# Performance work log

Measured on AMD Instinct MI355X. Metric: run time of the kernel, lower is better.

Reference implementation:

```python
import jax, jax.numpy as jnp
import numpy as np

B, C, E, H = 4, 2048, 1024, 16
D = E // H
EPS = 1e-5

def _layernorm(x, g, b):
    mu = jnp.mean(x, axis=-1, keepdims=True)
    var = jnp.mean(jnp.square(x - mu), axis=-1, keepdims=True)
    return (x - mu) * jax.lax.rsqrt(var + EPS) * g + b

def setup_inputs() -> dict:
    key = jax.random.key(0)
    ks = jax.random.split(key, 12)
    s = 1.0 / np.sqrt(E)
    return {
        "inputs": jax.random.normal(ks[0], (B, C, E), dtype=jnp.float32),
        "Wq": jax.random.normal(ks[1], (E, E), dtype=jnp.float32) * s,
        "bq": jnp.zeros((E,), dtype=jnp.float32),
        "Wk": jax.random.normal(ks[2], (E, E), dtype=jnp.float32) * s,
        "bk": jnp.zeros((E,), dtype=jnp.float32),
        "Wv": jax.random.normal(ks[3], (E, E), dtype=jnp.float32) * s,
        "bv": jnp.zeros((E,), dtype=jnp.float32),
        "g1": jnp.ones((E,), dtype=jnp.float32),
        "beta1": jnp.zeros((E,), dtype=jnp.float32),
        "g2": jnp.ones((E,), dtype=jnp.float32),
        "beta2": jnp.zeros((E,), dtype=jnp.float32),
        "W1": jax.random.normal(ks[4], (E, 4 * E), dtype=jnp.float32) * s,
        "bm1": jnp.zeros((4 * E,), dtype=jnp.float32),
        "W2": jax.random.normal(ks[5], (4 * E, E), dtype=jnp.float32) * (1.0 / np.sqrt(4 * E)),
        "bm2": jnp.zeros((E,), dtype=jnp.float32),
    }

def reference(inputs, Wq, bq, Wk, bk, Wv, bv, g1, beta1, g2, beta2, W1, bm1, W2, bm2):
    b, c, e = inputs.shape
    normed = _layernorm(inputs, g1, beta1)
    q = (normed @ Wq + bq).reshape(b, c, H, D).transpose(0, 2, 1, 3)  # [B,H,C,D]
    k = (normed @ Wk + bk).reshape(b, c, H, D).transpose(0, 2, 1, 3)
    v = (normed @ Wv + bv).reshape(b, c, H, D).transpose(0, 2, 1, 3)
    scores = jnp.einsum('bhqd,bhkd->bhqk', q, k) / np.sqrt(D).astype(np.float32)
    causal = jnp.triu(jnp.ones((c, c), dtype=bool), k=1)  # True above diagonal
    scores = jnp.where(causal, -jnp.inf, scores)
    probs = jax.nn.softmax(scores, axis=-1)
    attn = jnp.einsum('bhqk,bhkd->bhqd', probs, v)
    attn = attn.transpose(0, 2, 1, 3).reshape(b, c, e)
    out = inputs + attn
    h = _layernorm(out, g2, beta2)
    mlp = jax.nn.relu(h @ W1 + bm1) @ W2 + bm2
    return out + mlp
```

## Files before the change

kernel.cpp:

```cpp
#include <hip/hip_runtime.h>
#include <math.h>

#define B_ 4
#define C_ 2048
#define E_ 1024
#define H_ 16
#define D_ 64
#define ROWS_ (B_*C_)

typedef __bf16 bf16x8 __attribute__((ext_vector_type(8)));
typedef float f32x4 __attribute__((ext_vector_type(4)));

__device__ __forceinline__ float b2f(unsigned short u) {
  unsigned int x = ((unsigned int)u) << 16;
  return __builtin_bit_cast(float, x);
}
__device__ __forceinline__ unsigned short f2b(float f) {
  unsigned int x = __builtin_bit_cast(unsigned int, f);
  unsigned int r = (x + 0x7FFFu + ((x >> 16) & 1u)) >> 16;
  return (unsigned short)r;
}
__device__ __forceinline__ unsigned short tob(float f) { return f2b(f); }
__device__ __forceinline__ unsigned short tob(unsigned short u) { return u; }
__device__ __forceinline__ void store_out(float* p, float v) { *p = v; }
__device__ __forceinline__ void store_out(unsigned short* p, float v) { *p = f2b(v); }

__device__ __forceinline__ void async16(const void* g, void* l) {
  __builtin_amdgcn_global_load_lds(
      (__attribute__((address_space(1))) unsigned int*)g,
      (__attribute__((address_space(3))) unsigned int*)l, 16, 0, 0);
}

template <typename InT>
__global__ __launch_bounds__(256) void transpose64(
    const InT* __restrict__ in, unsigned short* __restrict__ out,
    int s_in, int s_out, int Hz, long zs_b, long zs_h, long zs_out)
{
  __shared__ unsigned short t[64][65];
  int z = blockIdx.z;
  long ib = (long)(z / Hz) * zs_b + (long)(z % Hz) * zs_h;
  long ob = (long)z * zs_out;
  int r0 = blockIdx.y * 64, c0 = blockIdx.x * 64;
  int lane = threadIdx.x & 63, grp = threadIdx.x >> 6;
  for (int i = grp; i < 64; i += 4)
    t[i][lane] = tob(in[ib + (long)(r0 + i) * s_in + c0 + lane]);
  __syncthreads();
  for (int i = grp; i < 64; i += 4)
    out[ob + (long)(c0 + i) * s_out + r0 + lane] = t[lane][i];
}

__global__ void concat_bias(const float* __restrict__ q,
                            const float* __restrict__ k,
                            const float* __restrict__ v,
                            float* __restrict__ o)
{
  int i = blockIdx.x * 256 + threadIdx.x;
  o[i] = (i < 1024) ? q[i] : (i < 2048) ? k[i - 1024] : v[i - 2048];
}

__global__ __launch_bounds__(256) void ln_kernel(
    const float* __restrict__ xin, const unsigned short* __restrict__ addend,
    const float* __restrict__ g, const float* __restrict__ beta,
    unsigned short* __restrict__ yout, float* __restrict__ out1)
{
  int row = blockIdx.x, tid = threadIdx.x;
  size_t base = (size_t)row * E_ + tid * 4;
  float4 xa = *(const float4*)(xin + base);
  float v0 = xa.x, v1 = xa.y, v2 = xa.z, v3 = xa.w;
  if (addend) {
    ushort4 aa = *(const ushort4*)(addend + base);
    v0 += b2f(aa.x); v1 += b2f(aa.y); v2 += b2f(aa.z); v3 += b2f(aa.w);
  }
  if (out1) {
    *(float4*)(out1 + base) = make_float4(v0, v1, v2, v3);
  }
  float s = v0 + v1 + v2 + v3;
  float sq = v0*v0 + v1*v1 + v2*v2 + v3*v3;
  #pragma unroll
  for (int off = 32; off >= 1; off >>= 1) {
    s  += __shfl_xor(s, off);
    sq += __shfl_xor(sq, off);
  }
  __shared__ float red[8];
  int wid = tid >> 6;
  if ((tid & 63) == 0) { red[wid] = s; red[4 + wid] = sq; }
  __syncthreads();
  s  = red[0] + red[1] + red[2] + red[3];
  sq = red[4] + red[5] + red[6] + red[7];
  float mu = s * (1.0f / E_);
  float var = sq * (1.0f / E_) - mu * mu;
  float rs = rsqrtf(var + 1e-5f);
  float4 ga = *(const float4*)(g + tid * 4);
  float4 ba = *(const float4*)(beta + tid * 4);
  ushort4 o;
  o.x = f2b((v0 - mu) * rs * ga.x + ba.x);
  o.y = f2b((v1 - mu) * rs * ga.y + ba.y);
  o.z = f2b((v2 - mu) * rs * ga.z + ba.z);
  o.w = f2b((v3 - mu) * rs * ga.w + ba.w);
  *(ushort4*)(yout + base) = o;
}

template <typename OutT>
__global__ __launch_bounds__(256) void gemm_bt(
    const unsigned short* __restrict__ A, const unsigned short* __restrict__ Bt,
    const float* __restrict__ bias, const float* __restrict__ resid,
    OutT* __restrict__ Co, int M, int N, int K, int relu)
{
  __shared__ __align__(16) unsigned short As[128 * 32];
  __shared__ __align__(16) unsigned short Bs[128 * 32];
  int tid = threadIdx.x, lane = tid & 63, wid = tid >> 6;
  int lane15 = lane & 15, quad = lane >> 4;
  int bn = blockIdx.x, bm = blockIdx.y;
  int m_lo = (wid & 1) * 64, n_lo = (wid >> 1) * 64;

  f32x4 acc[4][4];
  #pragma unroll
  for (int i = 0; i < 4; ++i)
    #pragma unroll
    for (int j = 0; j < 4; ++j) acc[i][j] = 0.0f;

  int c0 = wid * 64 + lane;
  int kc8 = (c0 & 3) * 8;
  const unsigned short* Ag0 = A  + (size_t)(bm * 128 + (c0 >> 2)) * K + kc8;
  const unsigned short* Ag1 = A  + (size_t)(bm * 128 + (c0 >> 2) + 64) * K + kc8;
  const unsigned short* Bg0 = Bt + (size_t)(bn * 128 + (c0 >> 2)) * K + kc8;
  const unsigned short* Bg1 = Bt + (size_t)(bn * 128 + (c0 >> 2) + 64) * K + kc8;
  unsigned short* As0 = &As[(wid * 64) * 8];
  unsigned short* As1 = &As[(256 + wid * 64) * 8];
  unsigned short* Bs0 = &Bs[(wid * 64) * 8];
  unsigned short* Bs1 = &Bs[(256 + wid * 64) * 8];

  for (int k0 = 0; k0 < K; k0 += 32) {
    async16(Ag0 + k0, As0);
    async16(Ag1 + k0, As1);
    async16(Bg0 + k0, Bs0);
    async16(Bg1 + k0, Bs1);
    __syncthreads();
    bf16x8 af[4], bfr[4];
    #pragma unroll
    for (int t = 0; t < 4; ++t)
      af[t] = *(const bf16x8*)&As[(m_lo + t * 16 + lane15) * 32 + quad * 8];
    #pragma unroll
    for (int t = 0; t < 4; ++t)
      bfr[t] = *(const bf16x8*)&Bs[(n_lo + t * 16 + lane15) * 32 + quad * 8];
    #pragma unroll
    for (int mt = 0; mt < 4; ++mt)
      #pragma unroll
      for (int nt = 0; nt < 4; ++nt)
        acc[mt][nt] = __builtin_amdgcn_mfma_f32_16x16x32_bf16(af[mt], bfr[nt], acc[mt][nt], 0, 0, 0);
    __syncthreads();
  }

  #pragma unroll
  for (int nt = 0; nt < 4; ++nt) {
    int col = bn * 128 + n_lo + nt * 16 + lane15;
    float bv = bias[col];
    #pragma unroll
    for (int mt = 0; mt < 4; ++mt) {
      int row0 = bm * 128 + m_lo + mt * 16 + quad * 4;
      #pragma unroll
      for (int r = 0; r < 4; ++r) {
        float val = acc[mt][nt][r] + bv;
        if (relu) val = fmaxf(val, 0.0f);
        if (resid) val += resid[(size_t)(row0 + r) * N + col];
        store_out(&Co[(size_t)(row0 + r) * N + col], val);
      }
    }
  }
}

__global__ __launch_bounds__(512) void attn_kernel(
    const unsigned short* __restrict__ qkv, const unsigned short* __restrict__ vt,
    unsigned short* __restrict__ attnb)
{
  __shared__ __align__(16) unsigned short Klds[64 * 64];
  __shared__ __align__(16) unsigned short Vlds[64 * 64];
  __shared__ __align__(16) unsigned short Plds[8][16 * 72];
  int tid = threadIdx.x, lane = tid & 63, widx = tid >> 6;
  int lane15 = lane & 15, quad = lane >> 4;
  int qblk = 15 - blockIdx.x;
  int bh = blockIdx.y;
  int b = bh >> 4, h = bh & 15;
  int q0w = qblk * 128 + widx * 16;

  const float QSCALE = 0.18033688011112042f;
  const unsigned short* qb = qkv + (size_t)(b * C_ + q0w + lane15) * 3072 + h * 64;
  bf16x8 qa0 = *(const bf16x8*)(qb + quad * 8);
  bf16x8 qa1 = *(const bf16x8*)(qb + 32 + quad * 8);
  #pragma unroll
  for (int j = 0; j < 8; ++j) {
    qa0[j] = (__bf16)((float)qa0[j] * QSCALE);
    qa1[j] = (__bf16)((float)qa1[j] * QSCALE);
  }

  float lsum[4];
  f32x4 o[4];
  #pragma unroll
  for (int r = 0; r < 4; ++r) lsum[r] = 0.0f;
  #pragma unroll
  for (int nt = 0; nt < 4; ++nt) o[nt] = 0.0f;

  int sr = tid >> 3, sc = tid & 7, sw = sr & 7;
  const unsigned short* kg = qkv + (size_t)(b * C_ + sr) * 3072 + 1024 + h * 64 + (sc ^ sw) * 8;
  const unsigned short* vg = vt + (size_t)bh * 64 * 2048 + (size_t)sr * 2048 + (sc ^ sw) * 8;
  unsigned short* kl = &Klds[sr * 64 + sc * 8];
  unsigned short* vl = &Vlds[sr * 64 + sc * 8];
  int swr = lane15 & 7;

  int ntiles = 2 * qblk + 2;
  for (int kt = 0; kt < ntiles; ++kt) {
    int k0 = kt * 64;
    async16(kg, kl);
    async16(vg, vl);
    kg += (size_t)64 * 3072;
    vg += 64;
    __syncthreads();

    if (k0 <= q0w + 15) {
      f32x4 s[4];
      #pragma unroll
      for (int g = 0; g < 4; ++g) s[g] = 0.0f;
      #pragma unroll
      for (int g = 0; g < 4; ++g) {
        int row = g * 16 + lane15;
        bf16x8 kf0 = *(const bf16x8*)&Klds[row * 64 + ((quad ^ swr) * 8)];
        bf16x8 kf1 = *(const bf16x8*)&Klds[row * 64 + (((4 + quad) ^ swr) * 8)];
        s[g] = __builtin_amdgcn_mfma_f32_16x16x32_bf16(qa0, kf0, s[g], 0, 0, 0);
        s[g] = __builtin_amdgcn_mfma_f32_16x16x32_bf16(qa1, kf1, s[g], 0, 0, 0);
      }

      if (k0 + 63 > q0w) {
        #pragma unroll
        for (int g = 0; g < 4; ++g)
          #pragma unroll
          for (int r = 0; r < 4; ++r)
            if (k0 + g * 16 + lane15 > q0w + quad * 4 + r) s[g][r] = -3.0e38f;
      }

      float p[4][4];
      #pragma unroll
      for (int g = 0; g < 4; ++g)
        #pragma unroll
        for (int r = 0; r < 4; ++r) p[g][r] = exp2f(s[g][r]);
      #pragma unroll
      for (int r = 0; r < 4; ++r)
        lsum[r] += (p[0][r] + p[1][r]) + (p[2][r] + p[3][r]);

      __bf16* prow = (__bf16*)&Plds[widx][0];
      #pragma unroll
      for (int g = 0; g < 4; ++g)
        #pragma unroll
        for (int r = 0; r < 4; ++r)
          prow[(quad * 4 + r) * 72 + g * 16 + lane15] = (__bf16)p[g][r];
      asm volatile("s_waitcnt lgkmcnt(0)" ::: "memory");
      bf16x8 pa0 = *(const bf16x8*)&Plds[widx][lane15 * 72 + quad * 8];
      bf16x8 pa1 = *(const bf16x8*)&Plds[widx][lane15 * 72 + 32 + quad * 8];

      #pragma unroll
      for (int nt = 0; nt < 4; ++nt) {
        int d = nt * 16 + lane15;
        bf16x8 vf0 = *(const bf16x8*)&Vlds[d * 64 + ((quad ^ swr) * 8)];
        bf16x8 vf1 = *(const bf16x8*)&Vlds[d * 64 + (((4 + quad) ^ swr) * 8)];
        o[nt] = __builtin_amdgcn_mfma_f32_16x16x32_bf16(pa0, vf0, o[nt], 0, 0, 0);
        o[nt] = __builtin_amdgcn_mfma_f32_16x16x32_bf16(pa1, vf1, o[nt], 0, 0, 0);
      }
    }
    __syncthreads();
  }

  #pragma unroll
  for (int off = 1; off <= 8; off <<= 1)
    #pragma unroll
    for (int r = 0; r < 4; ++r)
      lsum[r] += __shfl_xor(lsum[r], off);
  float rl[4];
  #pragma unroll
  for (int r = 0; r < 4; ++r) rl[r] = 1.0f / lsum[r];

  #pragma unroll
  for (int nt = 0; nt < 4; ++nt) {
    #pragma unroll
    for (int r = 0; r < 4; ++r) {
      float val = o[nt][r] * rl[r];
      attnb[(size_t)(b * C_ + q0w + quad * 4 + r) * E_ + h * 64 + nt * 16 + lane15] = f2b(val);
    }
  }
}

extern "C" void kernel_launch(void* const* d_in, const int* in_sizes, int n_in,
                              void* d_out, int out_size, void* d_ws, size_t ws_size,
                              hipStream_t stream)
{
  const float* x   = (const float*)d_in[0];
  const float* Wq  = (const float*)d_in[1];
  const float* bq  = (const float*)d_in[2];
  const float* Wk  = (const float*)d_in[3];
  const float* bk  = (const float*)d_in[4];
  const float* Wv  = (const float*)d_in[5];
  const float* bv  = (const float*)d_in[6];
  const float* g1  = (const float*)d_in[7];
  const float* be1 = (const float*)d_in[8];
  const float* g2  = (const float*)d_in[9];
  const float* be2 = (const float*)d_in[10];
  const float* W1  = (const float*)d_in[11];
  const float* bm1 = (const float*)d_in[12];
  const float* W2  = (const float*)d_in[13];
  const float* bm2 = (const float*)d_in[14];

  char* ws = (char*)d_ws;
  unsigned short* norm1 = (unsigned short*)(ws + 0);
  unsigned short* wT    = (unsigned short*)(ws + 16777216);
  unsigned short* w1T   = (unsigned short*)(ws + 23068672);
  unsigned short* w2T   = (unsigned short*)(ws + 31457280);
  float*          biasq = (float*)(ws + 39845888);
  unsigned short* qkv   = (unsigned short*)(ws + 39858176);
  unsigned short* vtb   = (unsigned short*)(ws + 90189824);
  unsigned short* mid   = (unsigned short*)(ws + 39858176);
  unsigned short* attnb = (unsigned short*)(ws + 106967040);
  float*          out1  = (float*)(ws + 123744256);

  transpose64<float><<<dim3(16, 16, 1), 256, 0, stream>>>(Wq, wT,               1024, 1024, 1, 0, 0, 0);
  transpose64<float><<<dim3(16, 16, 1), 256, 0, stream>>>(Wk, wT + 1024 * 1024, 1024, 1024, 1, 0, 0, 0);
  transpose64<float><<<dim3(16, 16, 1), 256, 0, stream>>>(Wv, wT + 2048 * 1024, 1024, 1024, 1, 0, 0, 0);
  transpose64<float><<<dim3(64, 16, 1), 256, 0, stream>>>(W1, w1T, 4096, 1024, 1, 0, 0, 0);
  transpose64<float><<<dim3(16, 64, 1), 256, 0, stream>>>(W2, w2T, 1024, 4096, 1, 0, 0, 0);
  concat_bias<<<12, 256, 0, stream>>>(bq, bk, bv, biasq);

  ln_kernel<<<ROWS_, 256, 0, stream>>>(x, nullptr, g1, be1, norm1, nullptr);

  gemm_bt<unsigned short><<<dim3(24, 64), 256, 0, stream>>>(
      norm1, wT, biasq, nullptr, qkv, 8192, 3072, 1024, 0);

  transpose64<unsigned short><<<dim3(1, 32, 64), 256, 0, stream>>>(
      qkv + 2048, vtb, 3072, 2048, 16, (long)C_ * 3072, 64, (long)64 * 2048);

  attn_kernel<<<dim3(16, 64), 512, 0, stream>>>(qkv, vtb, attnb);

  ln_kernel<<<ROWS_, 256, 0, stream>>>(x, attnb, g2, be2, norm1, out1);

  gemm_bt<unsigned short><<<dim3(32, 64), 256, 0, stream>>>(
      norm1, w1T, bm1, nullptr, mid, 8192, 4096, 1024, 1);
  gemm_bt<float><<<dim3(8, 64), 256, 0, stream>>>(
      mid, w2T, bm2, out1, (float*)d_out, 8192, 1024, 4096, 0);
}
```

Baseline: 624.9 us.

## Widen GEMM K-tile to 64 with swizzled LDS, XCD-aware block mapping, split-K MLP2

The GEMM now stages 64-wide K slices per iteration instead of 32, which halves the number of barriers. Shared memory uses an XOR-swizzled layout to avoid bank conflicts on the fragment reads. Blocks are remapped so each XCD handles a contiguous group of M-tiles, improving L2 locality. The second MLP GEMM, which launched only 512 blocks, is split along K into two partial fp32 outputs so it fills more CUs, and a new combine kernel adds the partials, bias and residual, at the cost of extra fp32 traffic and one more launch.

Result: faster. 564.1 us (-9.7%).

```diff
diff --git a/kernel.cpp b/kernel.cpp
--- a/kernel.cpp
+++ b/kernel.cpp
@@ -104,57 +104,72 @@
 __global__ __launch_bounds__(256) void gemm_bt(
     const unsigned short* __restrict__ A, const unsigned short* __restrict__ Bt,
     const float* __restrict__ bias, const float* __restrict__ resid,
-    OutT* __restrict__ Co, int M, int N, int K, int relu)
-{
-  __shared__ __align__(16) unsigned short As[128 * 32];
-  __shared__ __align__(16) unsigned short Bs[128 * 32];
+    OutT* __restrict__ Co, int M, int N, int K, int lda, int ldb,
+    int relu, size_t zs)
+{
+  __shared__ __align__(16) unsigned short As[128 * 64];
+  __shared__ __align__(16) unsigned short Bs[128 * 64];
   int tid = threadIdx.x, lane = tid & 63, wid = tid >> 6;
   int lane15 = lane & 15, quad = lane >> 4;
-  int bn = blockIdx.x, bm = blockIdx.y;
+
+  int i = blockIdx.x;
+  int xcd = i & 7, s = i >> 3;
+  int bn = s >> 3;
+  int bm = xcd * 8 + (s & 7);
+  size_t koff = (size_t)blockIdx.z * K;
+  Co += (size_t)blockIdx.z * zs;
+
   int m_lo = (wid & 1) * 64, n_lo = (wid >> 1) * 64;
 
   f32x4 acc[4][4];
   #pragma unroll
-  for (int i = 0; i < 4; ++i)
-    #pragma unroll
-    for (int j = 0; j < 4; ++j) acc[i][j] = 0.0f;
-
-  int c0 = wid * 64 + lane;
-  int kc8 = (c0 & 3) * 8;
-  const unsigned short* Ag0 = A  + (size_t)(bm * 128 + (c0 >> 2)) * K + kc8;
-  const unsigned short* Ag1 = A  + (size_t)(bm * 128 + (c0 >> 2) + 64) * K + kc8;
-  const unsigned short* Bg0 = Bt + (size_t)(bn * 128 + (c0 >> 2)) * K + kc8;
-  const unsigned short* Bg1 = Bt + (size_t)(bn * 128 + (c0 >> 2) + 64) * K + kc8;
-  unsigned short* As0 = &As[(wid * 64) * 8];
-  unsigned short* As1 = &As[(256 + wid * 64) * 8];
-  unsigned short* Bs0 = &Bs[(wid * 64) * 8];
-  unsigned short* Bs1 = &Bs[(256 + wid * 64) * 8];
-
-  for (int k0 = 0; k0 < K; k0 += 32) {
-    async16(Ag0 + k0, As0);
-    async16(Ag1 + k0, As1);
-    async16(Bg0 + k0, Bs0);
-    async16(Bg1 + k0, Bs1);
+  for (int a = 0; a < 4; ++a)
+    #pragma unroll
+    for (int bb = 0; bb < 4; ++bb) acc[a][bb] = 0.0f;
+
+  int sr = tid >> 3, sc = tid & 7;
+  int scs = (sc ^ (sr & 7)) * 8;
+  const unsigned short* Ag = A + koff + (size_t)(bm * 128 + sr) * lda + scs;
+  const unsigned short* Bg = Bt + koff + (size_t)(bn * 128 + sr) * ldb + scs;
+  unsigned short* Al = &As[wid * 512];
+  unsigned short* Bl = &Bs[wid * 512];
+  int sw15 = lane15 & 7;
+
+  for (int k0 = 0; k0 < K; k0 += 64) {
+    async16(Ag,                     Al);
+    async16(Ag + (size_t)32 * lda,  Al + 32 * 64);
+    async16(Ag + (size_t)64 * lda,  Al + 64 * 64);
+    async16(Ag + (size_t)96 * lda,  Al + 96 * 64);
+    async16(Bg,                     Bl);
+    async16(Bg + (size_t)32 * ldb,  Bl + 32 * 64);
+    async16(Bg + (size_t)64 * ldb,  Bl + 64 * 64);
+    async16(Bg + (size_t)96 * ldb,  Bl + 96 * 64);
+    Ag += 64; Bg += 64;
     __syncthreads();
-    bf16x8 af[4], bfr[4];
-    #pragma unroll
-    for (int t = 0; t < 4; ++t)
-      af[t] = *(const bf16x8*)&As[(m_lo + t * 16 + lane15) * 32 + quad * 8];
-    #pragma unroll
-    for (int t = 0; t < 4; ++t)
-      bfr[t] = *(const bf16x8*)&Bs[(n_lo + t * 16 + lane15) * 32 + quad * 8];
-    #pragma unroll
-    for (int mt = 0; mt < 4; ++mt)
-      #pragma unroll
-      for (int nt = 0; nt < 4; ++nt)
-        acc[mt][nt] = __builtin_amdgcn_mfma_f32_16x16x32_bf16(af[mt], bfr[nt], acc[mt][nt], 0, 0, 0);
+
+    #pragma unroll
+    for (int kk = 0; kk < 2; ++kk) {
+      bf16x8 af[4], bfr[4];
+      int qs = kk * 4 + quad;
+      #pragma unroll
+      for (int t = 0; t < 4; ++t)
+        af[t] = *(const bf16x8*)&As[(m_lo + t * 16 + lane15) * 64 + ((qs ^ sw15) * 8)];
+      #pragma unroll
+      for (int t = 0; t < 4; ++t)
+        bfr[t] = *(const bf16x8*)&Bs[(n_lo + t * 16 + lane15) * 64 + ((qs ^ sw15) * 8)];
+      #pragma unroll
+      for (int mt = 0; mt < 4; ++mt)
+        #pragma unroll
+        for (int nt = 0; nt < 4; ++nt)
+          acc[mt][nt] = __builtin_amdgcn_mfma_f32_16x16x32_bf16(af[mt], bfr[nt], acc[mt][nt], 0, 0, 0);
+    }
     __syncthreads();
   }
 
   #pragma unroll
   for (int nt = 0; nt < 4; ++nt) {
     int col = bn * 128 + n_lo + nt * 16 + lane15;
-    float bv = bias[col];
+    float bv = bias ? bias[col] : 0.0f;
     #pragma unroll
     for (int mt = 0; mt < 4; ++mt) {
       int row0 = bm * 128 + m_lo + mt * 16 + quad * 4;
@@ -167,6 +182,22 @@
       }
     }
   }
+}
+
+__global__ __launch_bounds__(256) void combine2(
+    const float* __restrict__ p0, const float* __restrict__ p1,
+    const float* __restrict__ resid, const float* __restrict__ bias,
+    float* __restrict__ out)
+{
+  int row = blockIdx.x, tid = threadIdx.x;
+  size_t base = (size_t)row * E_ + tid * 4;
+  float4 a = *(const float4*)(p0 + base);
+  float4 b = *(const float4*)(p1 + base);
+  float4 r = *(const float4*)(resid + base);
+  float4 bi = *(const float4*)(bias + tid * 4);
+  float4 o = make_float4(a.x + b.x + r.x + bi.x, a.y + b.y + r.y + bi.y,
+                         a.z + b.z + r.z + bi.z, a.w + b.w + r.w + bi.w);
+  *(float4*)(out + base) = o;
 }
 
 __global__ __launch_bounds__(512) void attn_kernel(
@@ -308,16 +339,19 @@
   const float* bm2 = (const float*)d_in[14];
 
   char* ws = (char*)d_ws;
+  float*          part0 = (float*)(ws + 0);
   unsigned short* norm1 = (unsigned short*)(ws + 0);
   unsigned short* wT    = (unsigned short*)(ws + 16777216);
   unsigned short* w1T   = (unsigned short*)(ws + 23068672);
-  unsigned short* w2T   = (unsigned short*)(ws + 31457280);
   float*          biasq = (float*)(ws + 39845888);
   unsigned short* qkv   = (unsigned short*)(ws + 39858176);
   unsigned short* vtb   = (unsigned short*)(ws + 90189824);
   unsigned short* mid   = (unsigned short*)(ws + 39858176);
   unsigned short* attnb = (unsigned short*)(ws + 106967040);
   float*          out1  = (float*)(ws + 123744256);
+  unsigned short* w2T   = (unsigned short*)(ws + 157298688);
+  float*          part1 = (float*)(ws + 165687296);
+  size_t part_zs = ((size_t)165687296) / 4;
 
   transpose64<float><<<dim3(16, 16, 1), 256, 0, stream>>>(Wq, wT,               1024, 1024, 1, 0, 0, 0);
   transpose64<float><<<dim3(16, 16, 1), 256, 0, stream>>>(Wk, wT + 1024 * 1024, 1024, 1024, 1, 0, 0, 0);
@@ -328,8 +362,8 @@
 
   ln_kernel<<<ROWS_, 256, 0, stream>>>(x, nullptr, g1, be1, norm1, nullptr);
 
-  gemm_bt<unsigned short><<<dim3(24, 64), 256, 0, stream>>>(
-      norm1, wT, biasq, nullptr, qkv, 8192, 3072, 1024, 0);
+  gemm_bt<unsigned short><<<dim3(24 * 64, 1, 1), 256, 0, stream>>>(
+      norm1, wT, biasq, nullptr, qkv, 8192, 3072, 1024, 1024, 1024, 0, 0);
 
   transpose64<unsigned short><<<dim3(1, 32, 64), 256, 0, stream>>>(
       qkv + 2048, vtb, 3072, 2048, 16, (long)C_ * 3072, 64, (long)64 * 2048);
@@ -338,8 +372,10 @@
 
   ln_kernel<<<ROWS_, 256, 0, stream>>>(x, attnb, g2, be2, norm1, out1);
 
-  gemm_bt<unsigned short><<<dim3(32, 64), 256, 0, stream>>>(
-      norm1, w1T, bm1, nullptr, mid, 8192, 4096, 1024, 1);
-  gemm_bt<float><<<dim3(8, 64), 256, 0, stream>>>(
-      mid, w2T, bm2, out1, (float*)d_out, 8192, 1024, 4096, 0);
-}
+  gemm_bt<unsigned short><<<dim3(32 * 64, 1, 1), 256, 0, stream>>>(
+      norm1, w1T, bm1, nullptr, mid, 8192, 4096, 1024, 1024, 1024, 1, 0);
+
+  gemm_bt<float><<<dim3(8 * 64, 1, 2), 256, 0, stream>>>(
+      mid, w2T, nullptr, nullptr, part0, 8192, 1024, 2048, 4096, 4096, 0, part_zs);
+  combine2<<<ROWS_, 256, 0, stream>>>(part0, part1, out1, bm2, (float*)d_out);
+}
```
